# Kernel tuning notes

Measured on AMD Instinct MI355X. Metric: run time of the kernel, lower is better.

Reference implementation:

```python
import jax, jax.numpy as jnp
import numpy as np
from jax import lax

B, NF, NOBJ, SZ = 16, 4, 32, 128
HALF = SZ // 2  # 64


def _build_grid(h, w):
    ys = jnp.linspace(0.0, 1.0, h)
    xs = jnp.linspace(0.0, 1.0, w)
    gy, gx = jnp.meshgrid(ys, xs, indexing='ij')
    g = jnp.stack([gy, gx], axis=-1)  # (H, W, 2)
    return jnp.concatenate([g, 1.0 - g], axis=-1)[None]  # (1, H, W, 4)


def setup_inputs() -> dict:
    key = jax.random.key(0)
    ks = jax.random.split(key, 8)
    images = jax.random.normal(ks[0], (B, 3 * NF, SZ, SZ), dtype=jnp.float32)
    rois = jax.random.randint(ks[1], (B, NOBJ, SZ, SZ), 0, 2).astype(jnp.bool_)
    conv1_w = jax.random.normal(ks[2], (64, 3 * NF, 3, 3), dtype=jnp.float32) * 0.05
    conv1_b = jnp.zeros((64,), dtype=jnp.float32)
    conv2_w = jax.random.normal(ks[3], (128, 64, 3, 3), dtype=jnp.float32) * 0.05
    conv2_b = jnp.zeros((128,), dtype=jnp.float32)
    dense_w = jax.random.normal(ks[4], (128, 4), dtype=jnp.float32) * 0.1
    dense_b = jnp.zeros((128,), dtype=jnp.float32)
    return dict(images=images, rois=rois, conv1_w=conv1_w, conv1_b=conv1_b,
                conv2_w=conv2_w, conv2_b=conv2_b, dense_w=dense_w, dense_b=dense_b)


def _conv(x, w, b):
    y = lax.conv_general_dilated(x, w, window_strides=(1, 1), padding='SAME',
                                 dimension_numbers=('NCHW', 'OIHW', 'NCHW'))
    return y + b[None, :, None, None]


def reference(images, rois, conv1_w, conv1_b, conv2_w, conv2_b, dense_w, dense_b):
    # conv stack
    x = jax.nn.relu(_conv(images, conv1_w, conv1_b))
    x = lax.reduce_window(x, -jnp.inf, lax.max, (1, 1, 2, 2), (1, 1, 2, 2), 'VALID')
    x = jax.nn.relu(_conv(x, conv2_w, conv2_b))  # (B, 128, 64, 64)
    # soft position embed
    grid = _build_grid(HALF, HALF)  # (1, 64, 64, 4)
    pe = grid @ dense_w.T + dense_b  # (1, 64, 64, 128)
    x = x + jnp.transpose(pe, (0, 3, 1, 2))  # (B, 128, 64, 64)
    # roi pool: nearest-downsample masks 128->64 (indices 0,2,4,...)
    r = rois[:, :, ::2, ::2].astype(x.dtype)  # (B, O, 64, 64)
    masked = x[:, None] * r[:, :, None]  # (B, O, 128, 64, 64)
    return jnp.max(masked, axis=(-2, -1))  # (B, O, 128)
```

## Files before the change

kernel.cpp:

```cpp
#include <hip/hip_runtime.h>


typedef __attribute__((ext_vector_type(8))) short short8;
typedef __attribute__((ext_vector_type(4))) float f32x4;
typedef __attribute__((ext_vector_type(4))) unsigned short us4;
typedef __attribute__((ext_vector_type(2))) unsigned short u16x2;
typedef unsigned short u16;
typedef unsigned int u32;

__device__ __forceinline__ u16 f2bf(float f) {
  u32 u = __builtin_bit_cast(u32, f);
  return (u16)((u + 0x7fffu + ((u >> 16) & 1u)) >> 16);
}
__device__ __forceinline__ u32 pkmaxu(u32 a, u32 b) {
  u16x2 x = __builtin_bit_cast(u16x2, a), y = __builtin_bit_cast(u16x2, b);
  return __builtin_bit_cast(u32, __builtin_elementwise_max(x, y));
}
__device__ __forceinline__ u32 map2(u32 v) {
  u32 flip = ((v & 0x80008000u) >> 15) * 0xFFFFu;
  return v ^ (flip | 0x80008000u);
}
__device__ __forceinline__ float unmap1(u32 m) {
  u32 b = m ^ ((m & 0x8000u) ? 0x8000u : 0xFFFFu);
  return __builtin_bit_cast(float, b << 16);
}

namespace {

__global__ __launch_bounds__(256) void kiop(const float* __restrict__ img,
                                            u16* __restrict__ imgT,
                                            const unsigned* __restrict__ rois,
                                            unsigned* __restrict__ rmask,
                                            const float* __restrict__ w2,
                                            u16* __restrict__ Aw2,
                                            const float* __restrict__ w1,
                                            u16* __restrict__ Aw1) {
  __shared__ alignas(16) u16 ST[2048];
  const int bx = blockIdx.x;
  const int t = threadIdx.x;
  if (bx < 2048) {
    const int row = bx & 127, b = bx >> 7;
#pragma unroll
    for (int i = 0; i < 2; ++i) {
      const int e = i * 256 + t;
      ST[(e >> 2) * 16 + 12 + (e & 3)] = 0;
    }
#pragma unroll
    for (int i = 0; i < 6; ++i) {
      const int e = i * 256 + t;
      const int ci = e >> 7, col = e & 127;
      const float v = img[(((size_t)(b * 12 + ci)) << 14) + row * 128 + col];
      ST[col * 16 + ci] = f2bf(v);
    }
    __syncthreads();
    us4* dst = (us4*)(imgT + (((size_t)(b * 128 + row)) << 11));
#pragma unroll
    for (int i = 0; i < 2; ++i) {
      const int q = i * 256 + t;
      dst[q] = *(const us4*)&ST[q * 4];
    }
  } else if (bx < 2176) {
    const int lane = t & 63;
    u32 ok = 1u;
#pragma unroll
    for (int i = 0; i < 4; ++i) {
      u32 v = rois[lane * 4 + i];
      ok &= ((v <= 1u) || (v == 0x3f800000u)) ? 1u : 0u;
    }
    const bool isWord = (__all((int)ok) != 0);
    const unsigned char* roisB = (const unsigned char*)rois;
    const int pi = (bx - 2048) * 256 + t;
    const int b = pi >> 11;
    const int pp = pi & 2047;
    const int h = pp >> 5;
    const int wp = pp & 31;
    const size_t base = (size_t)b * 32 * 16384 + (size_t)(2 * h) * 128 + 4 * wp;
    u32 m0 = 0, m1 = 0;
#pragma unroll
    for (int o = 0; o < 32; ++o) {
      const size_t idx = base + (size_t)o * 16384;
      if (isWord) {
        const uint4 q = *(const uint4*)&rois[idx];
        m0 |= (u32)(q.x != 0u) << o;
        m1 |= (u32)(q.z != 0u) << o;
      } else {
        const u32 q = *(const u32*)&roisB[idx];
        m0 |= (u32)((q & 0xffu) != 0u) << o;
        m1 |= (u32)((q & 0xff0000u) != 0u) << o;
      }
    }
    *(uint2*)&rmask[b * 4096 + h * 64 + wp * 2] = make_uint2(m0, m1);
  } else if (bx < 2464) {
    const int idx = (bx - 2176) * 256 + t;
    const int j = idx & 7;
    const int lane = (idx >> 3) & 63;
    const int t3 = idx >> 9;
    const int ks = t3 % 18, cot = t3 / 18;
    const int m = lane & 15, g = lane >> 4;
    const int co = cot * 16 + m;
    const int k = ks * 32 + g * 8 + j;
    const int rc = k >> 6, ci = k & 63;
    Aw2[idx] = f2bf(w2[co * 576 + ci * 9 + rc]);
  } else {
    const int idx = (bx - 2464) * 256 + t;
    const int j = idx & 7;
    const int lane = (idx >> 3) & 63;
    const int t3 = idx >> 9;
    const int ks = t3 % 5, cot = t3 / 5;
    const int m = lane & 15, g = lane >> 4;
    const int co = cot * 16 + m;
    const int k = ks * 32 + g * 8 + j;
    const int rc = k >> 4, cip = k & 15;
    const float v = (rc < 9 && cip < 12) ? w1[co * 108 + cip * 9 + rc] : 0.f;
    Aw1[idx] = f2bf(v);
  }
}

__global__ __launch_bounds__(256) void k1_mfma(const u16* __restrict__ imgT,
                                               const u16* __restrict__ Aw1,
                                               const float* __restrict__ b1,
                                               u16* __restrict__ pooledT) {
  __shared__ alignas(16) u16 SIMG[8192];
  __shared__ alignas(16) u16 PT[64 * 68];
  const int h2 = blockIdx.x, b = blockIdx.y;
  const int t = threadIdx.x, wv = t >> 6, l = t & 63;

#pragma unroll
  for (int i = 0; i < 4; ++i) {
    const int q = i * 256 + t;
    const int sr = q >> 8, off = q & 255;
    const int irow = 2 * h2 - 1 + sr;
    short8 v = {0, 0, 0, 0, 0, 0, 0, 0};
    if ((unsigned)irow < 128u)
      v = *(const short8*)(imgT + (((size_t)(b * 128 + irow)) << 11) + off * 8);
    *(short8*)((char*)SIMG + ((q * 16) ^ (((q >> 3) & 1) << 4))) = v;
  }
  __syncthreads();

  const int m16 = l & 15, g = l >> 4;
  const int colhalf = wv >> 1, cotbase = (wv & 1) * 2;
  const int cipb = (g & 1) * 16;
  f32x4 acc[2][8];
#pragma unroll
  for (int ct = 0; ct < 2; ++ct)
#pragma unroll
    for (int pt = 0; pt < 8; ++pt) acc[ct][pt] = (f32x4){0.f, 0.f, 0.f, 0.f};

  const u16* awb = Aw1 + (size_t)l * 8;
  const short8 z8 = {0, 0, 0, 0, 0, 0, 0, 0};

#pragma unroll
  for (int ks = 0; ks < 5; ++ks) {
    short8 a0 = *(const short8*)(awb + (cotbase * 5 + ks) * 512);
    short8 a1 = *(const short8*)(awb + ((cotbase + 1) * 5 + ks) * 512);
    const bool pz = (ks == 4) && (g >= 2);
    const int rc = pz ? 0 : (2 * ks + (g >> 1));
    const int rr = (rc * 11) >> 5;
    const int cc = rc - rr * 3;
    const int d = m16 - 1 + cc;
    const int sb = (d < 0) ? 1 : ((d >> 2) & 1);
    const int base = rr * 4096 + d * 32 + colhalf * 2048 + (cipb ^ (sb << 4));
    const bool killLo = (cc == 0) && (m16 == 0) && (colhalf == 0);
    const bool killHi = (cc == 2) && (m16 == 15) && (colhalf == 1);
#pragma unroll
    for (int pt = 0; pt < 8; ++pt) {
      const int r01 = pt >> 2, ct2 = pt & 3;
      short8 bv = *(const short8*)((const char*)SIMG + base + r01 * 4096 + ct2 * 512);
      bool kill = pz;
      if (ct2 == 0) kill = kill || killLo;
      if (ct2 == 3) kill = kill || killHi;
      if (kill) bv = z8;
      acc[0][pt] = __builtin_amdgcn_mfma_f32_16x16x32_bf16(a0, bv, acc[0][pt], 0, 0, 0);
      acc[1][pt] = __builtin_amdgcn_mfma_f32_16x16x32_bf16(a1, bv, acc[1][pt], 0, 0, 0);
    }
  }

#pragma unroll
  for (int ct = 0; ct < 2; ++ct) {
    const int cot = cotbase + ct;
#pragma unroll
    for (int r = 0; r < 4; ++r) {
      const int co = cot * 16 + g * 4 + r;
      const float bias = b1[co];
#pragma unroll
      for (int ct2 = 0; ct2 < 4; ++ct2) {
        float v0 = fmaxf(acc[ct][ct2][r] + bias, 0.f);
        float v1 = fmaxf(acc[ct][4 + ct2][r] + bias, 0.f);
        float vv = fmaxf(v0, v1);
        vv = fmaxf(vv, __shfl_xor(vv, 1, 64));
        if (!(m16 & 1)) {
          const int pw = colhalf * 32 + ct2 * 8 + (m16 >> 1);
          PT[pw * 68 + co] = f2bf(vv);
        }
      }
    }
  }
  __syncthreads();
  u16* dst = pooledT + (((size_t)(b * 64 + h2)) << 12);
#pragma unroll
  for (int i = 0; i < 4; ++i) {
    const int e = (i * 256 + t) * 4;
    const int pw = e >> 6, co = e & 63;
    *(us4*)(dst + e) = *(const us4*)&PT[pw * 68 + co];
  }
}

__global__ __launch_bounds__(256) void k2f(const u16* __restrict__ pooledT,
                                           const u16* __restrict__ Aw,
                                           const float* __restrict__ b2,
                                           const float* __restrict__ dw,
                                           const float* __restrict__ db,
                                           const unsigned* __restrict__ rmask,
                                           u32* __restrict__ partial) {
  __shared__ alignas(16) char SB[32768];
  __shared__ u32 MS[128];
  const int hp = blockIdx.x, b = blockIdx.y;
  const int t = threadIdx.x, wv = t >> 6, l = t & 63;

#pragma unroll
  for (int i = 0; i < 8; ++i) {
    const int chunk = i * 4 + wv;
    const int row = chunk >> 3;
    const int hin = 2 * hp - 1 + row;
    short8 v = {0, 0, 0, 0, 0, 0, 0, 0};
    if ((unsigned)hin < 64u)
      v = *(const short8*)(pooledT + (((size_t)(b * 64 + hin)) << 12) +
                           ((chunk & 7) << 9) + l * 8);
    const int lin = chunk * 1024 + l * 16;
    *(short8*)(SB + (lin ^ (((lin >> 7) & 7) << 4))) = v;
  }
  if (t < 128) MS[t] = rmask[b * 4096 + hp * 128 + t];
  __syncthreads();

  const int m16 = l & 15, g = l >> 4;
  const int kbyte = g * 16;
  f32x4 acc[2][8];
#pragma unroll
  for (int ct = 0; ct < 2; ++ct)
#pragma unroll
    for (int n = 0; n < 8; ++n) acc[ct][n] = (f32x4){0.f, 0.f, 0.f, 0.f};

  const u16* aw0 = Aw + (size_t)wv * 36 * 512 + l * 8;
  const short8 z8 = {0, 0, 0, 0, 0, 0, 0, 0};

#pragma unroll
  for (int ks = 0; ks < 18; ++ks) {
    const int rc = ks >> 1, r = rc / 3, c = rc % 3;
    const int koff = r * 8192 + (ks & 1) * 64 + kbyte;
    short8 a0 = *(const short8*)(aw0 + ks * 512);
    short8 a1 = *(const short8*)(aw0 + (18 + ks) * 512);
    const int d = m16 + c - 1;
    const int base = (koff + d * 128) ^ ((d & 7) << 4);
    const bool edgeLo = (c == 0) && (m16 == 0);
    const bool edgeHi = (c == 2) && (m16 == 15);
#pragma unroll
    for (int n = 0; n < 8; ++n) {
      const int orw = n >> 2, n4 = n & 3;
      short8 bv = *(const short8*)(SB + base + orw * 8192 + n4 * 2048);
      if (c == 0 && n4 == 0) { if (edgeLo) bv = z8; }
      if (c == 2 && n4 == 3) { if (edgeHi) bv = z8; }
      acc[0][n] = __builtin_amdgcn_mfma_f32_16x16x32_bf16(a0, bv, acc[0][n], 0, 0, 0);
      acc[1][n] = __builtin_amdgcn_mfma_f32_16x16x32_bf16(a1, bv, acc[1][n], 0, 0, 0);
    }
  }

  __syncthreads();

  const float inv63 = 1.f / 63.f;
#pragma unroll
  for (int ct = 0; ct < 2; ++ct) {
    const int cot = wv * 2 + ct;
#pragma unroll
    for (int r2 = 0; r2 < 2; ++r2) {
      const int co0 = cot * 16 + g * 4 + r2 * 2;
      const float bias0 = b2[co0], bias1 = b2[co0 + 1];
      const float pA0 = dw[co0 * 4 + 0] - dw[co0 * 4 + 2];
      const float pB0 = dw[co0 * 4 + 1] - dw[co0 * 4 + 3];
      const float pC0 = dw[co0 * 4 + 2] + dw[co0 * 4 + 3] + db[co0];
      const float pA1 = dw[co0 * 4 + 4] - dw[co0 * 4 + 6];
      const float pB1 = dw[co0 * 4 + 5] - dw[co0 * 4 + 7];
      const float pC1 = dw[co0 * 4 + 6] + dw[co0 * 4 + 7] + db[co0 + 1];
#pragma unroll
      for (int orw = 0; orw < 2; ++orw) {
        const float gy = (float)(2 * hp + orw) * inv63;
        const float pe00 = gy * pA0 + pC0;
        const float pe01 = gy * pA1 + pC1;
#pragma unroll
        for (int n4 = 0; n4 < 4; ++n4) {
          const int w = n4 * 16 + m16;
          const int pos = orw * 64 + w;
          const float gx = (float)w * inv63;
          const float v0 = fmaxf(acc[ct][orw * 4 + n4][r2 * 2 + 0] + bias0, 0.f)
                           + pe00 + gx * pB0;
          const float v1 = fmaxf(acc[ct][orw * 4 + n4][r2 * 2 + 1] + bias1, 0.f)
                           + pe01 + gx * pB1;
          const u32 pk = map2((u32)f2bf(v0) | ((u32)f2bf(v1) << 16));
          *(u32*)(SB + ((pos * 256 + co0 * 2) ^ ((pos & 7) << 4))) = pk;
        }
      }
    }
  }
  __syncthreads();

  const int og = t >> 5, coq = t & 31;
  u32 a0[4], a1[4];
#pragma unroll
  for (int r = 0; r < 4; ++r) { a0[r] = 0u; a1[r] = 0u; }
  for (int pos = 0; pos < 128; ++pos) {
    const u32 mw = MS[pos];
    const uint2 x = *(const uint2*)(SB + ((pos * 256 + coq * 8) ^ ((pos & 7) << 4)));
#pragma unroll
    for (int r = 0; r < 4; ++r) {
      const int o = og * 4 + r;
      const u32 am = (u32)((int)(mw << (31 - o)) >> 31);
      a0[r] = pkmaxu(a0[r], (x.x & am) | (0x80008000u & ~am));
      a1[r] = pkmaxu(a1[r], (x.y & am) | (0x80008000u & ~am));
    }
  }
  u32* pslab = partial + (size_t)hp * 32768;
#pragma unroll
  for (int r = 0; r < 4; ++r) {
    const int o = og * 4 + r;
    *(uint2*)&pslab[((b * 32 + o) << 6) + coq * 2] = make_uint2(a0[r], a1[r]);
  }
}

__global__ __launch_bounds__(256) void k4_merge(const u32* __restrict__ partial,
                                                float* __restrict__ out) {
  const int idx = blockIdx.x * 256 + threadIdx.x;
  u32 v = partial[idx];
#pragma unroll
  for (int q = 1; q < 32; ++q) v = pkmaxu(v, partial[q * 32768 + idx]);
  float2 o2;
  o2.x = unmap1(v & 0xFFFFu);
  o2.y = unmap1(v >> 16);
  *(float2*)&out[idx * 2] = o2;
}

}

extern "C" void kernel_launch(void* const* d_in, const int* in_sizes, int n_in,
                              void* d_out, int out_size, void* d_ws, size_t ws_size,
                              hipStream_t stream) {
  const float* images = (const float*)d_in[0];
  const unsigned* rois = (const unsigned*)d_in[1];
  const float* w1 = (const float*)d_in[2];
  const float* b1 = (const float*)d_in[3];
  const float* w2 = (const float*)d_in[4];
  const float* b2 = (const float*)d_in[5];
  const float* dw = (const float*)d_in[6];
  const float* db = (const float*)d_in[7];
  float* out = (float*)d_out;

  char* ws = (char*)d_ws;
  unsigned* rmask = (unsigned*)(ws);
  u16* pooledT = (u16*)(ws + 0x40000);
  u16* Aw2 = (u16*)(ws + 0x840000);
  u16* Aw1 = (u16*)(ws + 0x864000);
  u16* imgT = (u16*)(ws + 0x900000);
  u32* partial = (u32*)(ws + 0x900000);

  hipLaunchKernelGGL(kiop, dim3(2504), dim3(256), 0, stream,
                     images, imgT, rois, rmask, w2, Aw2, w1, Aw1);
  hipLaunchKernelGGL(k1_mfma, dim3(64, 16), dim3(256), 0, stream, imgT, Aw1, b1, pooledT);
  hipLaunchKernelGGL(k2f, dim3(32, 16), dim3(256), 0, stream,
                     pooledT, Aw2, b2, dw, db, rmask, partial);
  hipLaunchKernelGGL(k4_merge, dim3(128), dim3(256), 0, stream, partial, out);
}
```

Measured before the change: 64.29 us.

## Fuse image transpose into conv1 and overlap weight/mask prep blocks

New measurement: 66.80 us. 3.9% more time.

```diff
diff --git a/kernel.cpp b/kernel.cpp
--- a/kernel.cpp
+++ b/kernel.cpp
@@ -27,113 +27,106 @@
 
 namespace {
 
-__global__ __launch_bounds__(256) void kiop(const float* __restrict__ img,
-                                            u16* __restrict__ imgT,
-                                            const unsigned* __restrict__ rois,
-                                            unsigned* __restrict__ rmask,
-                                            const float* __restrict__ w2,
-                                            u16* __restrict__ Aw2,
-                                            const float* __restrict__ w1,
-                                            u16* __restrict__ Aw1) {
-  __shared__ alignas(16) u16 ST[2048];
+__global__ __launch_bounds__(256) void kw1(const float* __restrict__ w1,
+                                           u16* __restrict__ Aw1) {
+  const int idx = blockIdx.x * 256 + threadIdx.x;
+  const int j = idx & 7;
+  const int lane = (idx >> 3) & 63;
+  const int t3 = idx >> 9;
+  const int ks = t3 % 5, cot = t3 / 5;
+  const int m = lane & 15, g = lane >> 4;
+  const int co = cot * 16 + m;
+  const int k = ks * 32 + g * 8 + j;
+  const int rc = k >> 4, cip = k & 15;
+  const float v = (rc < 9 && cip < 12) ? w1[co * 108 + cip * 9 + rc] : 0.f;
+  Aw1[idx] = f2bf(v);
+}
+
+__global__ __launch_bounds__(256) void k1_mfma(const float* __restrict__ img,
+                                               const u16* __restrict__ Aw1,
+                                               const float* __restrict__ b1,
+                                               u16* __restrict__ pooledT,
+                                               const float* __restrict__ w2,
+                                               u16* __restrict__ Aw2,
+                                               const unsigned* __restrict__ rois,
+                                               unsigned* __restrict__ rmask) {
+  __shared__ alignas(16) u16 SIMG[8192];
+  __shared__ alignas(16) u16 PT[64 * 68];
   const int bx = blockIdx.x;
   const int t = threadIdx.x;
-  if (bx < 2048) {
-    const int row = bx & 127, b = bx >> 7;
-#pragma unroll
-    for (int i = 0; i < 2; ++i) {
-      const int e = i * 256 + t;
-      ST[(e >> 2) * 16 + 12 + (e & 3)] = 0;
-    }
-#pragma unroll
-    for (int i = 0; i < 6; ++i) {
-      const int e = i * 256 + t;
-      const int ci = e >> 7, col = e & 127;
-      const float v = img[(((size_t)(b * 12 + ci)) << 14) + row * 128 + col];
-      ST[col * 16 + ci] = f2bf(v);
-    }
-    __syncthreads();
-    us4* dst = (us4*)(imgT + (((size_t)(b * 128 + row)) << 11));
-#pragma unroll
-    for (int i = 0; i < 2; ++i) {
-      const int q = i * 256 + t;
-      dst[q] = *(const us4*)&ST[q * 4];
-    }
-  } else if (bx < 2176) {
-    const int lane = t & 63;
-    u32 ok = 1u;
-#pragma unroll
-    for (int i = 0; i < 4; ++i) {
-      u32 v = rois[lane * 4 + i];
-      ok &= ((v <= 1u) || (v == 0x3f800000u)) ? 1u : 0u;
-    }
-    const bool isWord = (__all((int)ok) != 0);
-    const unsigned char* roisB = (const unsigned char*)rois;
-    const int pi = (bx - 2048) * 256 + t;
-    const int b = pi >> 11;
-    const int pp = pi & 2047;
-    const int h = pp >> 5;
-    const int wp = pp & 31;
-    const size_t base = (size_t)b * 32 * 16384 + (size_t)(2 * h) * 128 + 4 * wp;
-    u32 m0 = 0, m1 = 0;
-#pragma unroll
-    for (int o = 0; o < 32; ++o) {
-      const size_t idx = base + (size_t)o * 16384;
-      if (isWord) {
-        const uint4 q = *(const uint4*)&rois[idx];
-        m0 |= (u32)(q.x != 0u) << o;
-        m1 |= (u32)(q.z != 0u) << o;
-      } else {
-        const u32 q = *(const u32*)&roisB[idx];
-        m0 |= (u32)((q & 0xffu) != 0u) << o;
-        m1 |= (u32)((q & 0xff0000u) != 0u) << o;
+
+  if (bx >= 1024) {
+    if (bx < 1312) {
+      const int idx = (bx - 1024) * 256 + t;
+      const int j = idx & 7;
+      const int lane = (idx >> 3) & 63;
+      const int t3 = idx >> 9;
+      const int ks = t3 % 18, cot = t3 / 18;
+      const int m = lane & 15, g = lane >> 4;
+      const int co = cot * 16 + m;
+      const int k = ks * 32 + g * 8 + j;
+      const int rc = k >> 6, ci = k & 63;
+      Aw2[idx] = f2bf(w2[co * 576 + ci * 9 + rc]);
+    } else {
+      const int lane = t & 63;
+      u32 ok = 1u;
+#pragma unroll
+      for (int i = 0; i < 4; ++i) {
+        u32 v = rois[lane * 4 + i];
+        ok &= ((v <= 1u) || (v == 0x3f800000u)) ? 1u : 0u;
       }
-    }
-    *(uint2*)&rmask[b * 4096 + h * 64 + wp * 2] = make_uint2(m0, m1);
-  } else if (bx < 2464) {
-    const int idx = (bx - 2176) * 256 + t;
-    const int j = idx & 7;
-    const int lane = (idx >> 3) & 63;
-    const int t3 = idx >> 9;
-    const int ks = t3 % 18, cot = t3 / 18;
-    const int m = lane & 15, g = lane >> 4;
-    const int co = cot * 16 + m;
-    const int k = ks * 32 + g * 8 + j;
-    const int rc = k >> 6, ci = k & 63;
-    Aw2[idx] = f2bf(w2[co * 576 + ci * 9 + rc]);
-  } else {
-    const int idx = (bx - 2464) * 256 + t;
-    const int j = idx & 7;
-    const int lane = (idx >> 3) & 63;
-    const int t3 = idx >> 9;
-    const int ks = t3 % 5, cot = t3 / 5;
-    const int m = lane & 15, g = lane >> 4;
-    const int co = cot * 16 + m;
-    const int k = ks * 32 + g * 8 + j;
-    const int rc = k >> 4, cip = k & 15;
-    const float v = (rc < 9 && cip < 12) ? w1[co * 108 + cip * 9 + rc] : 0.f;
-    Aw1[idx] = f2bf(v);
-  }
-}
-
-__global__ __launch_bounds__(256) void k1_mfma(const u16* __restrict__ imgT,
-                                               const u16* __restrict__ Aw1,
-                                               const float* __restrict__ b1,
-                                               u16* __restrict__ pooledT) {
-  __shared__ alignas(16) u16 SIMG[8192];
-  __shared__ alignas(16) u16 PT[64 * 68];
-  const int h2 = blockIdx.x, b = blockIdx.y;
-  const int t = threadIdx.x, wv = t >> 6, l = t & 63;
-
-#pragma unroll
-  for (int i = 0; i < 4; ++i) {
-    const int q = i * 256 + t;
-    const int sr = q >> 8, off = q & 255;
+      const bool isWord = (__all((int)ok) != 0);
+      const unsigned char* roisB = (const unsigned char*)rois;
+      const int pi = (bx - 1312) * 256 + t;
+      const int b = pi >> 11;
+      const int pp = pi & 2047;
+      const int h = pp >> 5;
+      const int wp = pp & 31;
+      const size_t base = (size_t)b * 32 * 16384 + (size_t)(2 * h) * 128 + 4 * wp;
+      u32 m0 = 0, m1 = 0;
+#pragma unroll
+      for (int o = 0; o < 32; ++o) {
+        const size_t idx = base + (size_t)o * 16384;
+        if (isWord) {
+          const uint4 q = *(const uint4*)&rois[idx];
+          m0 |= (u32)(q.x != 0u) << o;
+          m1 |= (u32)(q.z != 0u) << o;
+        } else {
+          const u32 q = *(const u32*)&roisB[idx];
+          m0 |= (u32)((q & 0xffu) != 0u) << o;
+          m1 |= (u32)((q & 0xff0000u) != 0u) << o;
+        }
+      }
+      *(uint2*)&rmask[b * 4096 + h * 64 + wp * 2] = make_uint2(m0, m1);
+    }
+    return;
+  }
+
+  const int h2 = bx & 63, b = bx >> 6;
+  const int wv = t >> 6, l = t & 63;
+
+#pragma unroll
+  for (int i = 0; i < 2; ++i) {
+    const int unit = i * 256 + t;
+    const int sr = unit >> 7, col = unit & 127;
+    const int lin = sr * 4096 + col * 32 + 24;
+    *(uint2*)((char*)SIMG + (lin ^ (((col >> 2) & 1) << 4))) = make_uint2(0u, 0u);
+  }
+#pragma unroll
+  for (int i = 0; i < 6; ++i) {
+    const int unit = i * 256 + t;
+    const int pair = unit >> 7;
+    const int col = unit & 127;
+    const int sr = pair / 3, q = pair % 3;
     const int irow = 2 * h2 - 1 + sr;
-    short8 v = {0, 0, 0, 0, 0, 0, 0, 0};
-    if ((unsigned)irow < 128u)
-      v = *(const short8*)(imgT + (((size_t)(b * 128 + irow)) << 11) + off * 8);
-    *(short8*)((char*)SIMG + ((q * 16) ^ (((q >> 3) & 1) << 4))) = v;
+    u32 lo = 0u, hi = 0u;
+    if ((unsigned)irow < 128u) {
+      const float* p = img + (((size_t)(b * 12 + q * 4)) << 14) + irow * 128 + col;
+      lo = (u32)f2bf(p[0]) | ((u32)f2bf(p[1 << 14]) << 16);
+      hi = (u32)f2bf(p[2 << 14]) | ((u32)f2bf(p[3 << 14]) << 16);
+    }
+    const int lin = sr * 4096 + col * 32 + q * 8;
+    *(uint2*)((char*)SIMG + (lin ^ (((col >> 2) & 1) << 4))) = make_uint2(lo, hi);
   }
   __syncthreads();
 
@@ -357,12 +350,11 @@
   u16* pooledT = (u16*)(ws + 0x40000);
   u16* Aw2 = (u16*)(ws + 0x840000);
   u16* Aw1 = (u16*)(ws + 0x864000);
-  u16* imgT = (u16*)(ws + 0x900000);
   u32* partial = (u32*)(ws + 0x900000);
 
-  hipLaunchKernelGGL(kiop, dim3(2504), dim3(256), 0, stream,
-                     images, imgT, rois, rmask, w2, Aw2, w1, Aw1);
-  hipLaunchKernelGGL(k1_mfma, dim3(64, 16), dim3(256), 0, stream, imgT, Aw1, b1, pooledT);
+  hipLaunchKernelGGL(kw1, dim3(40), dim3(256), 0, stream, w1, Aw1);
+  hipLaunchKernelGGL(k1_mfma, dim3(1440), dim3(256), 0, stream,
+                     images, Aw1, b1, pooledT, w2, Aw2, rois, rmask);
   hipLaunchKernelGGL(k2f, dim3(32, 16), dim3(256), 0, stream,
                      pooledT, Aw2, b2, dw, db, rmask, partial);
   hipLaunchKernelGGL(k4_merge, dim3(128), dim3(256), 0, stream, partial, out);
```

## Fuse final max-merge into conv2 kernel via last-block atomic counter

Applied to the files above, without the earlier changes.

Result: slower. 139.3 us (+116.7%).

```diff
diff --git a/kernel.cpp b/kernel.cpp
--- a/kernel.cpp
+++ b/kernel.cpp
@@ -34,7 +34,8 @@
                                             const float* __restrict__ w2,
                                             u16* __restrict__ Aw2,
                                             const float* __restrict__ w1,
-                                            u16* __restrict__ Aw1) {
+                                            u16* __restrict__ Aw1,
+                                            u32* __restrict__ counter) {
   __shared__ alignas(16) u16 ST[2048];
   const int bx = blockIdx.x;
   const int t = threadIdx.x;
@@ -60,6 +61,7 @@
       dst[q] = *(const us4*)&ST[q * 4];
     }
   } else if (bx < 2176) {
+    if (bx == 2048 && t < 16) counter[t] = 0;
     const int lane = t & 63;
     u32 ok = 1u;
 #pragma unroll
@@ -211,9 +213,12 @@
                                            const float* __restrict__ dw,
                                            const float* __restrict__ db,
                                            const unsigned* __restrict__ rmask,
-                                           u32* __restrict__ partial) {
+                                           u32* __restrict__ partial,
+                                           u32* __restrict__ counter,
+                                           float* __restrict__ out) {
   __shared__ alignas(16) char SB[32768];
   __shared__ u32 MS[128];
+  __shared__ int lastFlag;
   const int hp = blockIdx.x, b = blockIdx.y;
   const int t = threadIdx.x, wv = t >> 6, l = t & 63;
 
@@ -323,18 +328,31 @@
     const int o = og * 4 + r;
     *(uint2*)&pslab[((b * 32 + o) << 6) + coq * 2] = make_uint2(a0[r], a1[r]);
   }
-}
-
-__global__ __launch_bounds__(256) void k4_merge(const u32* __restrict__ partial,
-                                                float* __restrict__ out) {
-  const int idx = blockIdx.x * 256 + threadIdx.x;
-  u32 v = partial[idx];
-#pragma unroll
-  for (int q = 1; q < 32; ++q) v = pkmaxu(v, partial[q * 32768 + idx]);
-  float2 o2;
-  o2.x = unmap1(v & 0xFFFFu);
-  o2.y = unmap1(v >> 16);
-  *(float2*)&out[idx * 2] = o2;
+
+  __threadfence();
+  __syncthreads();
+  if (t == 0) {
+    const u32 old = __hip_atomic_fetch_add(&counter[b], 1u, __ATOMIC_ACQ_REL,
+                                           __HIP_MEMORY_SCOPE_AGENT);
+    lastFlag = (old == 31u) ? 1 : 0;
+  }
+  __syncthreads();
+  if (lastFlag) {
+    __threadfence();
+    const u32* pb = partial + b * 2048;
+#pragma unroll
+    for (int i = 0; i < 8; ++i) {
+      const int cell = i * 256 + t;
+      u32 v = pb[cell];
+#pragma unroll
+      for (int q = 1; q < 32; ++q) v = pkmaxu(v, pb[q * 32768 + cell]);
+      const int o = cell >> 6, cp = cell & 63;
+      float2 o2;
+      o2.x = unmap1(v & 0xFFFFu);
+      o2.y = unmap1(v >> 16);
+      *(float2*)&out[((size_t)(b * 32 + o) << 7) + cp * 2] = o2;
+    }
+  }
 }
 
 }
@@ -357,13 +375,13 @@
   u16* pooledT = (u16*)(ws + 0x40000);
   u16* Aw2 = (u16*)(ws + 0x840000);
   u16* Aw1 = (u16*)(ws + 0x864000);
+  u32* counter = (u32*)(ws + 0x870000);
   u16* imgT = (u16*)(ws + 0x900000);
-  u32* partial = (u32*)(ws + 0x900000);
+  u32* partial = (u32*)(ws + 0xD00000);
 
   hipLaunchKernelGGL(kiop, dim3(2504), dim3(256), 0, stream,
-                     images, imgT, rois, rmask, w2, Aw2, w1, Aw1);
+                     images, imgT, rois, rmask, w2, Aw2, w1, Aw1, counter);
   hipLaunchKernelGGL(k1_mfma, dim3(64, 16), dim3(256), 0, stream, imgT, Aw1, b1, pooledT);
   hipLaunchKernelGGL(k2f, dim3(32, 16), dim3(256), 0, stream,
-                     pooledT, Aw2, b2, dw, db, rmask, partial);
-  hipLaunchKernelGGL(k4_merge, dim3(128), dim3(256), 0, stream, partial, out);
-}
+                     pooledT, Aw2, b2, dw, db, rmask, partial, counter, out);
+}
```
